# Kernel optimization log

Hardware: AMD Instinct MI355X
Metric: run time of the kernel (lower is better)

## Reference

```python
import jax, jax.numpy as jnp
import numpy as np

IN_CH, OUT_CH, K, STRIDE, PAD = 256, 256, 5, 1, 2


def setup_inputs() -> dict:
    key = jax.random.key(0)
    kx, kw = jax.random.split(key)
    x = jax.random.normal(kx, (32, IN_CH, 4096), dtype=jnp.float32)
    # kaiming_uniform_(a=sqrt(5)) -> bound = 1/sqrt(fan_in), fan_in = in_ch*k
    bound = 1.0 / np.sqrt(IN_CH * K)
    weight = jax.random.uniform(kw, (OUT_CH, IN_CH, K), dtype=jnp.float32,
                                minval=-bound, maxval=bound)
    bias = jnp.zeros((OUT_CH,), dtype=jnp.float32)
    return {"x": x, "weight": weight, "bias": bias}


def reference(x, weight, bias):
    # x: [B, C_in, W]; weight: [C_out, C_in, K] -> out: [B, C_out, W_out]
    out = jax.lax.conv_general_dilated(
        x, weight,
        window_strides=(STRIDE,),
        padding=[(PAD, PAD)],
        dimension_numbers=("NCH", "OIH", "NCH"),
    )
    return out + bias[None, :, None]
```

## Files before the change

kernel.cpp:

```cpp
#include <hip/hip_runtime.h>
#include <hip/hip_bf16.h>

typedef unsigned short u16;
typedef unsigned int u32;
typedef __attribute__((ext_vector_type(8))) short short8;
typedef __attribute__((ext_vector_type(4))) float floatx4;

#define NB 32
#define NCI 256
#define NCO 256
#define NW 4096
#define NK 5

#define WSTEP 16384
#define W2_BYTES (40 * WSTEP)

#define XROWB 64
#define XROWS 132
#define XBUF (XROWS * XROWB)
#define XSWZ(r) ((((r) >> 1) & 3) << 4)

#define FENCE asm volatile("" ::: "memory")
#define LK0   asm volatile("s_waitcnt lgkmcnt(0)" ::: "memory")


__global__ void wprep(const float* __restrict__ wgt, u16* __restrict__ W2) {
    int i = blockIdx.x * 256 + threadIdx.x;
    if (i >= NCO * NCI * NK) return;
    int k  = i % NK;
    int ci = (i / NK) % NCI;
    int co = i / (NCI * NK);
    int cb = ci >> 5, cr = ci & 31;
    __hip_bfloat16 h = __float2bfloat16(wgt[i]);
    W2[((size_t)(cb * NK + k) * 256 + co) * 32 + cr] = *reinterpret_cast<u16*>(&h);
}

__device__ __forceinline__ u16 bf16bits(float f) {
    __hip_bfloat16 h = __float2bfloat16(f);
    return *reinterpret_cast<u16*>(&h);
}


__global__ __launch_bounds__(512, 2)
void conv_mfma(const float* __restrict__ x, const u16* __restrict__ W2,
               const float* __restrict__ bias, float* __restrict__ out) {
    __shared__ __align__(16) char xlds[2 * XBUF];

    const int bid  = blockIdx.x;
    const int wt   = bid & 31;
    const int b    = bid >> 5;
    const int tid  = threadIdx.x;
    const int lane = tid & 63;
    const int wave = tid >> 6;
    const int wm   = wave >> 1;
    const int wn   = wave & 1;
    const int mrow = lane & 15;
    const int g    = lane >> 4;
    const int w0   = wt * 128;

    floatx4 acc[4][4];
#pragma unroll
    for (int mi = 0; mi < 4; ++mi)
#pragma unroll
        for (int ni = 0; ni < 4; ++ni)
            acc[mi][ni] = (floatx4){0.f, 0.f, 0.f, 0.f};

    const float* xb   = x + (size_t)b * NCI * NW;
    const char*  wimg = (const char*)W2;

    const int wloc = tid & 127;
    const int cig  = tid >> 7;
    const int soff = (2 + wloc) * XROWB + ((cig * 16) ^ XSWZ(2 + wloc));
    const float* xcol = xb + w0 + wloc;

    const int hidx = wave * 16 + (lane & 15);
    const int hri  = hidx >> 5;
    const int hci  = hidx & 31;
    const int hwg  = (hri < 2) ? (w0 - 2 + hri) : (w0 + 128 + (hri - 2));
    const int hwc  = (hwg < 0) ? 0 : ((hwg > NW - 1) ? (NW - 1) : hwg);
    const bool hok = (hwg >= 0) && (hwg < NW);
    const int hrloc = (hri < 2) ? hri : (130 + (hri - 2));
    const int hoff  = hrloc * XROWB + (((hci >> 3) ^ ((hrloc >> 1) & 3)) * 16) + (hci & 7) * 2;

    const int afrow = wm * 64 + mrow;

#define AFLOAD(dst, s_)                                                         \
    {                                                                           \
        const char* wt_ = wimg + (size_t)(s_) * WSTEP;                          \
        _Pragma("unroll")                                                       \
        for (int mi = 0; mi < 4; ++mi)                                          \
            dst[mi] = *(const short8*)(wt_ + (afrow + mi * 16) * 64 + g * 16);  \
    }

    short8 af[2][4];
    float v[8];
    float hvv = 0.f;

    {
        float v0[8];
#pragma unroll
        for (int j = 0; j < 8; ++j)
            v0[j] = xcol[(size_t)(cig * 8 + j) * NW];
        float hv0 = xb[(size_t)hci * NW + hwc];
        u32 p[4];
#pragma unroll
        for (int jp = 0; jp < 4; ++jp)
            p[jp] = (u32)bf16bits(v0[2 * jp]) | ((u32)bf16bits(v0[2 * jp + 1]) << 16);
        *(int4*)(xlds + soff) = *(int4*)p;
        if ((lane & 63) < 16)
            *(u16*)(xlds + hoff) = bf16bits(hok ? hv0 : 0.f);
#pragma unroll
        for (int j = 0; j < 8; ++j)
            v[j] = xcol[(size_t)(32 + cig * 8 + j) * NW];
        hvv = xb[(size_t)(32 + hci) * NW + hwc];
        AFLOAD(af[0], 0);
        LK0;
    }
    FENCE; __builtin_amdgcn_s_barrier(); FENCE;

#pragma unroll
    for (int cb = 0; cb < 8; ++cb) {
        const char* xcur = xlds + (cb & 1) * XBUF;
        char* xnxt       = xlds + ((cb + 1) & 1) * XBUF;
#pragma unroll
        for (int t = 0; t < NK; ++t) {
            const int s = cb * NK + t;
            if (s < 39)
                AFLOAD(af[(s + 1) & 1], s + 1);
            short8 bf[4];
#pragma unroll
            for (int ni = 0; ni < 4; ++ni) {
                int rx = wn * 64 + ni * 16 + mrow + t;
                bf[ni] = *(const short8*)(xcur + rx * XROWB + ((g * 16) ^ XSWZ(rx)));
            }
            __builtin_amdgcn_s_setprio(1);
#pragma unroll
            for (int mi = 0; mi < 4; ++mi)
#pragma unroll
                for (int ni = 0; ni < 4; ++ni)
                    acc[mi][ni] = __builtin_amdgcn_mfma_f32_16x16x32_bf16(
                        af[s & 1][mi], bf[ni], acc[mi][ni], 0, 0, 0);
            __builtin_amdgcn_s_setprio(0);
        }
        if (cb < 7) {
            u32 p[4];
#pragma unroll
            for (int jp = 0; jp < 4; ++jp)
                p[jp] = (u32)bf16bits(v[2 * jp]) | ((u32)bf16bits(v[2 * jp + 1]) << 16);
            *(int4*)(xnxt + soff) = *(int4*)p;
            if ((lane & 63) < 16)
                *(u16*)(xnxt + hoff) = bf16bits(hok ? hvv : 0.f);
            if (cb < 6) {
                const float* sx = xcol + (size_t)((cb + 2) * 32 + cig * 8) * NW;
#pragma unroll
                for (int j = 0; j < 8; ++j)
                    v[j] = sx[(size_t)j * NW];
                hvv = xb[(size_t)((cb + 2) * 32 + hci) * NW + hwc];
            }
            LK0;
            FENCE; __builtin_amdgcn_s_barrier(); FENCE;
        }
    }

#pragma unroll
    for (int mi = 0; mi < 4; ++mi) {
        int cobase = wm * 64 + mi * 16 + g * 4;
        float bv[4];
#pragma unroll
        for (int r = 0; r < 4; ++r) bv[r] = bias[cobase + r];
#pragma unroll
        for (int ni = 0; ni < 4; ++ni) {
            int col = w0 + wn * 64 + ni * 16 + mrow;
#pragma unroll
            for (int r = 0; r < 4; ++r)
                out[((size_t)b * NCO + cobase + r) * NW + col] =
                    acc[mi][ni][r] + bv[r];
        }
    }
#undef AFLOAD
}


__global__ void conv_naive(const float* __restrict__ x, const float* __restrict__ wgt,
                           const float* __restrict__ bias, float* __restrict__ out) {
    int w  = blockIdx.x * 256 + threadIdx.x;
    int co = blockIdx.y;
    int b  = blockIdx.z;
    float acc = bias[co];
    for (int ci = 0; ci < NCI; ci++) {
        const float* xr = x + ((size_t)b * NCI + ci) * NW;
        const float* wr = wgt + ((size_t)co * NCI + ci) * NK;
#pragma unroll
        for (int k = 0; k < NK; k++) {
            int wi = w + k - 2;
            if (wi >= 0 && wi < NW) acc += xr[wi] * wr[k];
        }
    }
    out[((size_t)b * NCO + co) * NW + w] = acc;
}


extern "C" void kernel_launch(void* const* d_in, const int* in_sizes, int n_in,
                              void* d_out, int out_size, void* d_ws, size_t ws_size,
                              hipStream_t stream) {
    const float* x    = (const float*)d_in[0];
    const float* wgt  = (const float*)d_in[1];
    const float* bias = (const float*)d_in[2];
    float* out        = (float*)d_out;

    if (ws_size < (size_t)W2_BYTES) {
        conv_naive<<<dim3(NW / 256, NCO, NB), 256, 0, stream>>>(x, wgt, bias, out);
        return;
    }

    u16* W2 = (u16*)d_ws;
    wprep<<<(NCO * NCI * NK + 255) / 256, 256, 0, stream>>>(wgt, W2);
    conv_mfma<<<1024, 512, 0, stream>>>(x, W2, bias, out);
}
```

Baseline: 119.1 us.

## Split output channels across two 256-thread blocks and restructure x prefetch

Each block now covers 128 output channels instead of 256, so the grid doubles to 2048 blocks of 256 threads, with launch bounds raised to 3 blocks per CU. Each thread stages 16 input channels per chunk instead of 8, and the global load for the next channel chunk now happens at the start of each iteration instead of two chunks ahead. The aim is better occupancy and load balance. The cost is that every x tile is loaded twice, once by each output-channel half, and the prefetch distance is shorter, so load latency may show.

```diff
diff --git a/kernel.cpp b/kernel.cpp
--- a/kernel.cpp
+++ b/kernel.cpp
@@ -41,14 +41,15 @@
 }
 
 
-__global__ __launch_bounds__(512, 2)
+__global__ __launch_bounds__(256, 3)
 void conv_mfma(const float* __restrict__ x, const u16* __restrict__ W2,
                const float* __restrict__ bias, float* __restrict__ out) {
     __shared__ __align__(16) char xlds[2 * XBUF];
 
     const int bid  = blockIdx.x;
-    const int wt   = bid & 31;
-    const int b    = bid >> 5;
+    const int cot  = bid & 1;
+    const int wt   = (bid >> 1) & 31;
+    const int b    = bid >> 6;
     const int tid  = threadIdx.x;
     const int lane = tid & 63;
     const int wave = tid >> 6;
@@ -70,49 +71,47 @@
 
     const int wloc = tid & 127;
     const int cig  = tid >> 7;
-    const int soff = (2 + wloc) * XROWB + ((cig * 16) ^ XSWZ(2 + wloc));
+    const int soff0 = (2 + wloc) * XROWB + ((cig * 32) ^ XSWZ(2 + wloc));
+    const int soff1 = (2 + wloc) * XROWB + ((cig * 32 + 16) ^ XSWZ(2 + wloc));
     const float* xcol = xb + w0 + wloc;
 
-    const int hidx = wave * 16 + (lane & 15);
-    const int hri  = hidx >> 5;
-    const int hci  = hidx & 31;
+    const int hri  = (tid >> 5) & 3;
+    const int hci  = tid & 31;
     const int hwg  = (hri < 2) ? (w0 - 2 + hri) : (w0 + 128 + (hri - 2));
     const int hwc  = (hwg < 0) ? 0 : ((hwg > NW - 1) ? (NW - 1) : hwg);
     const bool hok = (hwg >= 0) && (hwg < NW);
     const int hrloc = (hri < 2) ? hri : (130 + (hri - 2));
     const int hoff  = hrloc * XROWB + (((hci >> 3) ^ ((hrloc >> 1) & 3)) * 16) + (hci & 7) * 2;
-
-    const int afrow = wm * 64 + mrow;
-
-#define AFLOAD(dst, s_)                                                         \
-    {                                                                           \
-        const char* wt_ = wimg + (size_t)(s_) * WSTEP;                          \
-        _Pragma("unroll")                                                       \
-        for (int mi = 0; mi < 4; ++mi)                                          \
-            dst[mi] = *(const short8*)(wt_ + (afrow + mi * 16) * 64 + g * 16);  \
+    const bool hdo  = (tid < 128);
+
+    const int afrow = cot * 128 + wm * 64 + mrow;
+
+#define AFLOAD(dst, s_)                                                          \
+    {                                                                            \
+        const char* wt_ = wimg + (size_t)(s_) * WSTEP;                           \
+        _Pragma("unroll")                                                        \
+        for (int mi = 0; mi < 4; ++mi)                                           \
+            dst[mi] = *(const short8*)(wt_ + (afrow + mi * 16) * 64 + g * 16);   \
     }
 
     short8 af[2][4];
-    float v[8];
+    float v[16];
     float hvv = 0.f;
 
     {
-        float v0[8];
-#pragma unroll
-        for (int j = 0; j < 8; ++j)
-            v0[j] = xcol[(size_t)(cig * 8 + j) * NW];
+        float v0[16];
+#pragma unroll
+        for (int j = 0; j < 16; ++j)
+            v0[j] = xcol[(size_t)(cig * 16 + j) * NW];
         float hv0 = xb[(size_t)hci * NW + hwc];
-        u32 p[4];
-#pragma unroll
-        for (int jp = 0; jp < 4; ++jp)
+        u32 p[8];
+#pragma unroll
+        for (int jp = 0; jp < 8; ++jp)
             p[jp] = (u32)bf16bits(v0[2 * jp]) | ((u32)bf16bits(v0[2 * jp + 1]) << 16);
-        *(int4*)(xlds + soff) = *(int4*)p;
-        if ((lane & 63) < 16)
+        *(int4*)(xlds + soff0) = *(int4*)&p[0];
+        *(int4*)(xlds + soff1) = *(int4*)&p[4];
+        if (hdo)
             *(u16*)(xlds + hoff) = bf16bits(hok ? hv0 : 0.f);
-#pragma unroll
-        for (int j = 0; j < 8; ++j)
-            v[j] = xcol[(size_t)(32 + cig * 8 + j) * NW];
-        hvv = xb[(size_t)(32 + hci) * NW + hwc];
         AFLOAD(af[0], 0);
         LK0;
     }
@@ -122,6 +121,13 @@
     for (int cb = 0; cb < 8; ++cb) {
         const char* xcur = xlds + (cb & 1) * XBUF;
         char* xnxt       = xlds + ((cb + 1) & 1) * XBUF;
+        if (cb < 7) {
+            const float* sx = xcol + (size_t)((cb + 1) * 32 + cig * 16) * NW;
+#pragma unroll
+            for (int j = 0; j < 16; ++j)
+                v[j] = sx[(size_t)j * NW];
+            hvv = xb[(size_t)((cb + 1) * 32 + hci) * NW + hwc];
+        }
 #pragma unroll
         for (int t = 0; t < NK; ++t) {
             const int s = cb * NK + t;
@@ -143,20 +149,14 @@
             __builtin_amdgcn_s_setprio(0);
         }
         if (cb < 7) {
-            u32 p[4];
-#pragma unroll
-            for (int jp = 0; jp < 4; ++jp)
+            u32 p[8];
+#pragma unroll
+            for (int jp = 0; jp < 8; ++jp)
                 p[jp] = (u32)bf16bits(v[2 * jp]) | ((u32)bf16bits(v[2 * jp + 1]) << 16);
-            *(int4*)(xnxt + soff) = *(int4*)p;
-            if ((lane & 63) < 16)
+            *(int4*)(xnxt + soff0) = *(int4*)&p[0];
+            *(int4*)(xnxt + soff1) = *(int4*)&p[4];
+            if (hdo)
                 *(u16*)(xnxt + hoff) = bf16bits(hok ? hvv : 0.f);
-            if (cb < 6) {
-                const float* sx = xcol + (size_t)((cb + 2) * 32 + cig * 8) * NW;
-#pragma unroll
-                for (int j = 0; j < 8; ++j)
-                    v[j] = sx[(size_t)j * NW];
-                hvv = xb[(size_t)((cb + 2) * 32 + hci) * NW + hwc];
-            }
             LK0;
             FENCE; __builtin_amdgcn_s_barrier(); FENCE;
         }
@@ -164,17 +164,16 @@
 
 #pragma unroll
     for (int mi = 0; mi < 4; ++mi) {
-        int cobase = wm * 64 + mi * 16 + g * 4;
+        int cobase = cot * 128 + wm * 64 + mi * 16 + g * 4;
         float bv[4];
 #pragma unroll
         for (int r = 0; r < 4; ++r) bv[r] = bias[cobase + r];
 #pragma unroll
-        for (int ni = 0; ni < 4; ++ni) {
-            int col = w0 + wn * 64 + ni * 16 + mrow;
-#pragma unroll
-            for (int r = 0; r < 4; ++r)
-                out[((size_t)b * NCO + cobase + r) * NW + col] =
-                    acc[mi][ni][r] + bv[r];
+        for (int r = 0; r < 4; ++r) {
+            float* orow = out + ((size_t)b * NCO + cobase + r) * NW + w0 + wn * 64 + mrow;
+#pragma unroll
+            for (int ni = 0; ni < 4; ++ni)
+                orow[ni * 16] = acc[mi][ni][r] + bv[r];
         }
     }
 #undef AFLOAD
@@ -215,5 +214,5 @@
 
     u16* W2 = (u16*)d_ws;
     wprep<<<(NCO * NCI * NK + 255) / 256, 256, 0, stream>>>(wgt, W2);
-    conv_mfma<<<1024, 512, 0, stream>>>(x, W2, bias, out);
-}
+    conv_mfma<<<2048, 256, 0, stream>>>(x, W2, bias, out);
+}
```

Measured after the change: 290.3 us. 2.44x slower.
